# Kernel optimization log

Measured on AMD Instinct MI355X. Metric: run time of the kernel, lower is better.

The kernel has to match this reference:

```python
import jax, jax.numpy as jnp
import numpy as np

D = 1024      # model_size
H = 16        # n_heads
HD = D // H   # head_size
B = 8
S = 1024


def setup_inputs() -> dict:
    key = jax.random.key(0)
    ks = jax.random.split(key, 8)
    sq = lambda k, shp: jax.random.normal(k, shp, dtype=jnp.float32) * (1.0 / np.sqrt(shp[0]))
    return {
        "query": jax.random.normal(ks[0], (B, S, D), dtype=jnp.float32),
        "value": jax.random.normal(ks[1], (B, S, D), dtype=jnp.float32),
        "Wq": sq(ks[2], (D, D)),
        "bq": jnp.zeros((D,), dtype=jnp.float32),
        "Wkv": sq(ks[3], (D, 2 * D)),
        "bkv": jnp.zeros((2 * D,), dtype=jnp.float32),
        "Wo": sq(ks[4], (D, D)),
        "bo": jnp.zeros((D,), dtype=jnp.float32),
    }


def reference(query, value, Wq, bq, Wkv, bkv, Wo, bo):
    scale = 1.0 / jnp.sqrt(jnp.float32(HD))
    q = query @ Wq + bq                      # [B,S,D]
    kv = value @ Wkv + bkv                   # [B,S,2D]
    # tf.split(kv, 2H): chunks 0..H-1 are K heads, H..2H-1 are V heads
    k = kv[..., :D].reshape(B, S, H, HD)
    v = kv[..., D:].reshape(B, S, H, HD)
    qh = q.reshape(B, S, H, HD)
    scores = jnp.einsum("bqhd,bkhd->bhqk", qh, k) * scale   # [B,H,S,S]
    attn = jax.nn.softmax(scores, axis=-1)
    heads = jnp.einsum("bhqk,bkhd->bqhd", attn, v).reshape(B, S, D)
    return heads @ Wo + bo
```

## Files before the change

### kernel.cpp

```cpp
#include <hip/hip_runtime.h>
#include <math.h>

#define B_  8
#define S_  1024
#define D_  1024
#define H_  16
#define HD_ 64

typedef float          floatx4  __attribute__((ext_vector_type(4)));
typedef __bf16         bf16x8   __attribute__((ext_vector_type(8)));
typedef unsigned int   uintx2   __attribute__((ext_vector_type(2)));
typedef unsigned int   uintx4   __attribute__((ext_vector_type(4)));

__device__ __forceinline__ unsigned short f2bf(float f) {
    union { float f; unsigned u; } v; v.f = f;
    unsigned r = v.u + 0x7FFFu + ((v.u >> 16) & 1u);
    return (unsigned short)(r >> 16);
}
__device__ __forceinline__ unsigned pk2(float a, float b) {
    union { __bf16 h[2]; unsigned u; } r;
    r.h[0] = (__bf16)a; r.h[1] = (__bf16)b;
    return r.u;
}
__device__ __forceinline__ void async16(const void* g, void* l) {
    __builtin_amdgcn_global_load_lds(
        (__attribute__((address_space(1))) void*)g,
        (__attribute__((address_space(3))) void*)l, 16, 0, 0);
}

__global__ __launch_bounds__(256) void prep_k(const float* __restrict__ query,
                                              const float* __restrict__ value,
                                              unsigned short* __restrict__ qbf,
                                              unsigned short* __restrict__ vbf,
                                              const float* __restrict__ Wq,
                                              const float* __restrict__ Wkv,
                                              const float* __restrict__ Wo,
                                              unsigned short* __restrict__ WqT,
                                              unsigned short* __restrict__ WkvT,
                                              unsigned short* __restrict__ WoT) {
    __shared__ float T[64 * 68];
    const int t   = threadIdx.x;
    const int bid = blockIdx.x;
    if (bid < 8192) {
        int i = bid * 256 + t;
        floatx4 a = ((const floatx4*)query)[i];
        floatx4 b = ((const floatx4*)value)[i];
        uintx2 oa = { pk2(a[0], a[1]), pk2(a[2], a[3]) };
        uintx2 ob = { pk2(b[0], b[1]), pk2(b[2], b[3]) };
        ((uintx2*)qbf)[i] = oa;
        ((uintx2*)vbf)[i] = ob;
        return;
    }
    const int lin = bid - 8192;
    const int z   = lin >> 8;
    const float* W; unsigned short* WT; int Ndim, nbase;
    if (z == 0)      { W = Wq;  WT = WqT;  Ndim = 1024; nbase = 0; }
    else if (z == 3) { W = Wo;  WT = WoT;  Ndim = 1024; nbase = 0; }
    else             { W = Wkv; WT = WkvT; Ndim = 2048; nbase = (z - 1) * 1024; }
    const int n0 = (lin & 15) * 64 + nbase;
    const int k0 = ((lin >> 4) & 15) * 64;
#pragma unroll
    for (int rep = 0; rep < 4; ++rep) {
        int kl = (t >> 4) + rep * 16;
        int ns = (t & 15) * 4;
        *(floatx4*)(T + kl * 68 + ns) = *(const floatx4*)(W + (size_t)(k0 + kl) * Ndim + n0 + ns);
    }
    __syncthreads();
#pragma unroll
    for (int rep = 0; rep < 2; ++rep) {
        int nl = (t >> 3) + rep * 32;
        int ks = (t & 7) * 8;
        union { unsigned short s[8]; uintx4 u; } o;
#pragma unroll
        for (int j = 0; j < 8; ++j) o.s[j] = f2bf(T[(ks + j) * 68 + nl]);
        *(uintx4*)(WT + (size_t)(n0 + nl) * 1024 + k0 + ks) = o.u;
    }
}

template<int SWAP>
__device__ __forceinline__ void kloop(const unsigned short* __restrict__ ga0,
                                      const unsigned short* __restrict__ gb0,
                                      unsigned short* __restrict__ As,
                                      unsigned short* __restrict__ Bs,
                                      floatx4 (&acc)[4][4],
                                      int w, int lane) {
    const int quad = lane >> 4;
    const int l15  = lane & 15;
    const int e7   = l15 & 7;
    const int wr   = (w >> 1) * 64;
    const int wc   = (w & 1) * 64;
    for (int k0 = 0; k0 < 1024; k0 += 64) {
        if (k0) __syncthreads();
#pragma unroll
        for (int i = 0; i < 4; ++i) {
            int c = i * 4 + w;
            async16(ga0 + (size_t)(c * 8) * 1024 + k0, As + c * 512);
            async16(gb0 + (size_t)(c * 8) * 1024 + k0, Bs + c * 512);
        }
        __syncthreads();
#pragma unroll
        for (int ks = 0; ks < 2; ++ks) {
            bf16x8 af[4], bf[4];
#pragma unroll
            for (int mi = 0; mi < 4; ++mi)
                af[mi] = *(const bf16x8*)(As + (wr + mi * 16 + l15) * 64 + (((ks * 4 + quad) ^ e7) * 8));
#pragma unroll
            for (int ni = 0; ni < 4; ++ni)
                bf[ni] = *(const bf16x8*)(Bs + (wc + ni * 16 + l15) * 64 + (((ks * 4 + quad) ^ e7) * 8));
#pragma unroll
            for (int mi = 0; mi < 4; ++mi)
#pragma unroll
                for (int ni = 0; ni < 4; ++ni)
                    acc[mi][ni] = SWAP
                        ? __builtin_amdgcn_mfma_f32_16x16x32_bf16(bf[ni], af[mi], acc[mi][ni], 0, 0, 0)
                        : __builtin_amdgcn_mfma_f32_16x16x32_bf16(af[mi], bf[ni], acc[mi][ni], 0, 0, 0);
        }
    }
}

__global__ __launch_bounds__(256, 4) void qkv_gemm_k(const unsigned short* __restrict__ qbf,
                                                     const unsigned short* __restrict__ vbf,
                                                     const unsigned short* __restrict__ WqT,
                                                     const unsigned short* __restrict__ WkvT,
                                                     const float* __restrict__ bq,
                                                     const float* __restrict__ bkv,
                                                     unsigned short* __restrict__ Qb,
                                                     unsigned short* __restrict__ Kb,
                                                     unsigned short* __restrict__ Vtg,
                                                     float cexp) {
    __shared__ unsigned short SMEM[2 * 128 * 64];
    unsigned short* As = SMEM;
    unsigned short* Bs = SMEM + 128 * 64;
    const int t    = threadIdx.x;
    const int lane = t & 63;
    const int w    = t >> 6;
    const int quad = lane >> 4;
    const int l15  = lane & 15;
    const int wr   = (w >> 1) * 64;
    const int wc   = (w & 1) * 64;
    const int lrow = lane >> 3;
    const int lswz = ((lane & 7) ^ lrow) * 8;

    const int swz = (blockIdx.x & 7) * 192 + (blockIdx.x >> 3);
    int m0, n0;
    const unsigned short *Ap, *Wp;
    const float* bp;
    unsigned short* outp;
    float sc;
    bool vpath = false;
    if (swz < 512) {
        m0 = (swz >> 3) * 128; n0 = (swz & 7) * 128;
        Ap = qbf; Wp = WqT; bp = bq; outp = Qb; sc = cexp;
    } else {
        int b2 = swz - 512;
        m0 = (b2 >> 4) * 128; n0 = (b2 & 15) * 128;
        Ap = vbf; Wp = WkvT; bp = bkv; outp = Kb; sc = 1.0f;
        vpath = (n0 >= 1024);
    }

    floatx4 acc[4][4] = {};
    const unsigned short* ga0 = Ap + (size_t)(m0 + lrow) * 1024 + lswz;
    const unsigned short* gb0 = Wp + (size_t)(n0 + lrow) * 1024 + lswz;

    if (!vpath) {
        kloop<1>(ga0, gb0, As, Bs, acc, w, lane);
        __syncthreads();
#pragma unroll
        for (int hn = 0; hn < 2; ++hn) {
            if ((w & 1) == hn) {
#pragma unroll
                for (int ni = 0; ni < 4; ++ni) {
                    const int nb = n0 + wc + ni * 16 + quad * 4;
                    const floatx4 b4 = *(const floatx4*)(bp + nb);
#pragma unroll
                    for (int mi = 0; mi < 4; ++mi) {
                        const int ml = wr + mi * 16 + l15;
                        floatx4 v = acc[mi][ni];
                        uintx2 o = { pk2((v[0] + b4[0]) * sc, (v[1] + b4[1]) * sc),
                                     pk2((v[2] + b4[2]) * sc, (v[3] + b4[3]) * sc) };
                        *(uintx2*)(SMEM + ml * 72 + ni * 16 + quad * 4) = o;
                    }
                }
            }
            __syncthreads();
#pragma unroll
            for (int p = 0; p < 4; ++p) {
                int u   = p * 256 + t;
                int row = u >> 3, ch = u & 7;
                uintx4 x = *(const uintx4*)(SMEM + row * 72 + ch * 8);
                *(uintx4*)(outp + (size_t)(m0 + row) * 1024 + (n0 & 1023) + hn * 64 + ch * 8) = x;
            }
            __syncthreads();
        }
    } else {
        kloop<0>(ga0, gb0, As, Bs, acc, w, lane);
        const int c0 = n0 - 1024;
        const int s0 = m0 & 1023;
        const int bb = m0 >> 10;
        __syncthreads();
#pragma unroll
        for (int hc = 0; hc < 2; ++hc) {
            if ((w & 1) == hc) {
#pragma unroll
                for (int ni = 0; ni < 4; ++ni) {
                    const int rl = ni * 16 + l15;
                    const float bv = bp[n0 + wc + ni * 16 + l15];
#pragma unroll
                    for (int mi = 0; mi < 4; ++mi) {
                        const int sl = wr + mi * 16 + quad * 4;
                        floatx4 v = acc[mi][ni];
                        uintx2 o = { pk2(v[0] + bv, v[1] + bv), pk2(v[2] + bv, v[3] + bv) };
                        *(uintx2*)(SMEM + rl * 136 + sl) = o;
                    }
                }
            }
            __syncthreads();
#pragma unroll
            for (int p = 0; p < 4; ++p) {
                int u   = p * 256 + t;
                int row = u >> 4, ch = u & 15;
                uintx4 x = *(const uintx4*)(SMEM + row * 136 + ch * 8);
                *(uintx4*)(Vtg + ((size_t)(bb * 1024 + c0 + hc * 64 + row)) * 1024 + s0 + ch * 8) = x;
            }
            __syncthreads();
        }
    }
}

__global__ __launch_bounds__(256, 4) void o_gemm_k(const unsigned short* __restrict__ Hb,
                                                   const unsigned short* __restrict__ WoT,
                                                   const float* __restrict__ bo,
                                                   float* __restrict__ out) {
    __shared__ unsigned short As[128 * 64];
    __shared__ unsigned short Bs[128 * 64];
    const int t    = threadIdx.x;
    const int lane = t & 63;
    const int w    = t >> 6;
    const int quad = lane >> 4;
    const int l15  = lane & 15;
    const int wr   = (w >> 1) * 64;
    const int wc   = (w & 1) * 64;
    const int lrow = lane >> 3;
    const int lswz = ((lane & 7) ^ lrow) * 8;
    const int swz = (blockIdx.x & 7) * 64 + (blockIdx.x >> 3);
    const int m0  = (swz >> 3) * 128;
    const int n0  = (swz & 7) * 128;

    floatx4 acc[4][4] = {};
    const unsigned short* ga0 = Hb  + (size_t)(m0 + lrow) * 1024 + lswz;
    const unsigned short* gb0 = WoT + (size_t)(n0 + lrow) * 1024 + lswz;
    kloop<1>(ga0, gb0, As, Bs, acc, w, lane);

#pragma unroll
    for (int ni = 0; ni < 4; ++ni) {
        const int nb = n0 + wc + ni * 16 + quad * 4;
        const floatx4 b4 = *(const floatx4*)(bo + nb);
#pragma unroll
        for (int mi = 0; mi < 4; ++mi) {
            const int m = m0 + wr + mi * 16 + l15;
            floatx4 v = acc[mi][ni];
            floatx4 o = { v[0] + b4[0], v[1] + b4[1], v[2] + b4[2], v[3] + b4[3] };
            *(floatx4*)(out + (size_t)m * 1024 + nb) = o;
        }
    }
}

__global__ __launch_bounds__(512, 4) void attn_kernel(const unsigned short* __restrict__ Qb,
                                                      const unsigned short* __restrict__ Kb,
                                                      const unsigned short* __restrict__ Vtg,
                                                      unsigned short* __restrict__ Hb) {
    __shared__ unsigned short QPs[256 * 64];
    __shared__ unsigned short Ks[2][64 * 64];
    __shared__ unsigned short Vs[2][64 * 64];

    const int lin = blockIdx.x;
    const int xcd = lin & 7;
    const int grp = lin >> 3;
    const int bh  = xcd * 16 + (grp >> 2);
    const int qt  = grp & 3;
    const int b   = bh >> 4;
    const int h   = bh & 15;
    const int q0  = qt * 256;

    const int t    = threadIdx.x;
    const int lane = t & 63;
    const int w    = t >> 6;
    const int quad = lane >> 4;
    const int l15  = lane & 15;
    const int e7   = l15 & 7;
    const int lrow = lane >> 3;
    const int lswz = ((lane & 7) ^ lrow) * 8;

    {
        const unsigned short* gq = Qb + ((size_t)(b * S_ + q0)) * D_ + h * HD_;
#pragma unroll
        for (int i = 0; i < 4; ++i) {
            int r0 = (w * 4 + i) * 8;
            async16(gq + (size_t)(r0 + lrow) * D_ + lswz, QPs + r0 * 64);
        }
    }
    __syncthreads();

    bf16x8 bQ[2][2];
#pragma unroll
    for (int ks = 0; ks < 2; ++ks)
#pragma unroll
        for (int ni = 0; ni < 2; ++ni)
            bQ[ks][ni] = *(const bf16x8*)(QPs + (w * 32 + ni * 16 + l15) * 64 + ((ks * 4 + quad) ^ e7) * 8);

    const unsigned short* gkbase = Kb  + ((size_t)b * S_) * D_ + h * HD_;
    const unsigned short* gvbase = Vtg + ((size_t)(b * D_ + h * HD_)) * S_;

    float   lsum[2] = { 0.f, 0.f };
    floatx4 oacc[4][2] = {};
    unsigned short* Psw = QPs + w * (32 * 64);

    auto stageK = [&](int kt, int buf) {
        int r0 = w * 8;
        async16(gkbase + (size_t)(kt * 64 + r0 + lrow) * D_ + lswz, &Ks[buf][r0 * 64]);
    };
    auto stageV = [&](int kt, int buf) {
        int r0 = w * 8;
        async16(gvbase + (size_t)(r0 + lrow) * S_ + kt * 64 + lswz, &Vs[buf][r0 * 64]);
    };

    stageK(0, 0);
    stageV(0, 0);

#pragma unroll 1
    for (int kt = 0; kt < 16; ++kt) {
        const int cur = kt & 1;
        asm volatile("s_waitcnt vmcnt(0)\n\ts_barrier" ::: "memory");
        if (kt < 15) { stageK(kt + 1, cur ^ 1); stageV(kt + 1, cur ^ 1); }

        floatx4 st[4][2] = {};
#pragma unroll
        for (int ks = 0; ks < 2; ++ks) {
            bf16x8 aK[4];
#pragma unroll
            for (int mi = 0; mi < 4; ++mi)
                aK[mi] = *(const bf16x8*)(&Ks[cur][0] + (mi * 16 + l15) * 64 + ((ks * 4 + quad) ^ e7) * 8);
            __builtin_amdgcn_s_setprio(1);
#pragma unroll
            for (int mi = 0; mi < 4; ++mi)
#pragma unroll
                for (int ni = 0; ni < 2; ++ni)
                    st[mi][ni] = __builtin_amdgcn_mfma_f32_16x16x32_bf16(aK[mi], bQ[ks][ni], st[mi][ni], 0, 0, 0);
            __builtin_amdgcn_s_setprio(0);
        }

#pragma unroll
        for (int ni = 0; ni < 2; ++ni) {
            float ls = 0.f;
#pragma unroll
            for (int mi = 0; mi < 4; ++mi) {
                float p0 = __builtin_amdgcn_exp2f(st[mi][ni][0]);
                float p1 = __builtin_amdgcn_exp2f(st[mi][ni][1]);
                float p2 = __builtin_amdgcn_exp2f(st[mi][ni][2]);
                float p3 = __builtin_amdgcn_exp2f(st[mi][ni][3]);
                ls += (p0 + p1) + (p2 + p3);
                uintx2 pk = { pk2(p0, p1), pk2(p2, p3) };
                *(uintx2*)(Psw + (ni * 16 + l15) * 64 +
                           (((2 * mi + (quad >> 1)) ^ e7) * 8 + (quad & 1) * 4)) = pk;
            }
            lsum[ni] += ls;
        }

#pragma unroll
        for (int ks = 0; ks < 2; ++ks) {
            bf16x8 aV[4], bP[2];
#pragma unroll
            for (int mi = 0; mi < 4; ++mi)
                aV[mi] = *(const bf16x8*)(&Vs[cur][0] + (mi * 16 + l15) * 64 + ((ks * 4 + quad) ^ e7) * 8);
#pragma unroll
            for (int ni = 0; ni < 2; ++ni)
                bP[ni] = *(const bf16x8*)(Psw + (ni * 16 + l15) * 64 + ((ks * 4 + quad) ^ e7) * 8);
            __builtin_amdgcn_s_setprio(1);
#pragma unroll
            for (int mi = 0; mi < 4; ++mi)
#pragma unroll
                for (int ni = 0; ni < 2; ++ni)
                    oacc[mi][ni] = __builtin_amdgcn_mfma_f32_16x16x32_bf16(aV[mi], bP[ni], oacc[mi][ni], 0, 0, 0);
            __builtin_amdgcn_s_setprio(0);
        }
    }

    float rl[2];
#pragma unroll
    for (int ni = 0; ni < 2; ++ni) {
        float l = lsum[ni];
        l += __shfl_xor(l, 16);
        l += __shfl_xor(l, 32);
        rl[ni] = 1.f / l;
    }
#pragma unroll
    for (int mi = 0; mi < 4; ++mi)
#pragma unroll
        for (int ni = 0; ni < 2; ++ni) {
            uintx2 pk = { pk2(oacc[mi][ni][0] * rl[ni], oacc[mi][ni][1] * rl[ni]),
                          pk2(oacc[mi][ni][2] * rl[ni], oacc[mi][ni][3] * rl[ni]) };
            *(uintx2*)(Psw + (ni * 16 + l15) * 64 +
                       (((2 * mi + (quad >> 1)) ^ e7) * 8 + (quad & 1) * 4)) = pk;
        }
    {
        int qrow = lane >> 1;
        int kh   = lane & 1;
        size_t obase = ((size_t)(b * S_ + q0 + w * 32 + qrow)) * D_ + h * HD_ + kh * 32;
        int e = qrow & 7;
#pragma unroll
        for (int j = 0; j < 4; ++j) {
            int chunk = kh * 4 + j;
            *(uintx4*)(Hb + obase + j * 8) =
                *(const uintx4*)(Psw + qrow * 64 + ((chunk ^ e) * 8));
        }
    }
}

extern "C" void kernel_launch(void* const* d_in, const int* in_sizes, int n_in,
                              void* d_out, int out_size, void* d_ws, size_t ws_size,
                              hipStream_t stream) {
    (void)in_sizes; (void)n_in; (void)out_size; (void)ws_size;
    const float* query = (const float*)d_in[0];
    const float* value = (const float*)d_in[1];
    const float* Wq    = (const float*)d_in[2];
    const float* bq    = (const float*)d_in[3];
    const float* Wkv   = (const float*)d_in[4];
    const float* bkv   = (const float*)d_in[5];
    const float* Wo    = (const float*)d_in[6];
    const float* bo    = (const float*)d_in[7];

    const size_t MS = (size_t)B_ * S_;
    char* p = (char*)d_ws;
    unsigned short* qbf  = (unsigned short*)p; p += MS * D_ * 2;
    unsigned short* vbf  = (unsigned short*)p; p += MS * D_ * 2;
    unsigned short* WqT  = (unsigned short*)p; p += (size_t)D_ * D_ * 2;
    unsigned short* WkvT = (unsigned short*)p; p += (size_t)2 * D_ * D_ * 2;
    unsigned short* WoT  = (unsigned short*)p; p += (size_t)D_ * D_ * 2;
    unsigned short* Qb   = (unsigned short*)p; p += MS * D_ * 2;
    unsigned short* Kb   = (unsigned short*)p; p += MS * D_ * 2;
    unsigned short* Vtg  = (unsigned short*)p; p += MS * D_ * 2;
    unsigned short* Hb   = qbf;

    const float cexp = 0.125f * 1.44269504088896341f;

    prep_k<<<9216, 256, 0, stream>>>(query, value, qbf, vbf, Wq, Wkv, Wo, WqT, WkvT, WoT);
    qkv_gemm_k<<<1536, 256, 0, stream>>>(qbf, vbf, WqT, WkvT, bq, bkv, Qb, Kb, Vtg, cexp);
    attn_kernel<<<512, 512, 0, stream>>>(Qb, Kb, Vtg, Hb);
    o_gemm_k<<<512, 256, 0, stream>>>(Hb, WoT, bo, (float*)d_out);
}
```

Baseline: 262.8 us.

## Fuse fp32-to-bf16 activation cast into QKV GEMM A-tile loads

Drops the separate pass that casts query and value to bf16. The QKV GEMM now reads fp32 activations directly and converts them in registers before writing the A tile to LDS, so the bf16 copies are never written out and read back. The block-to-tile mapping also changes from a swizzled order to m-fastest ordering in both GEMMs. The trade-off is that the A-tile load becomes a synchronous register load plus conversion instead of an async global-to-LDS copy, and each A tile is fetched from global memory at twice the byte size, once per N tile.

Measured after the change: 267.6 us. No clear change (+1.8%).

```diff
diff --git a/kernel.cpp b/kernel.cpp
--- a/kernel.cpp
+++ b/kernel.cpp
@@ -28,11 +28,7 @@
         (__attribute__((address_space(3))) void*)l, 16, 0, 0);
 }
 
-__global__ __launch_bounds__(256) void prep_k(const float* __restrict__ query,
-                                              const float* __restrict__ value,
-                                              unsigned short* __restrict__ qbf,
-                                              unsigned short* __restrict__ vbf,
-                                              const float* __restrict__ Wq,
+__global__ __launch_bounds__(256) void prep_k(const float* __restrict__ Wq,
                                               const float* __restrict__ Wkv,
                                               const float* __restrict__ Wo,
                                               unsigned short* __restrict__ WqT,
@@ -40,18 +36,7 @@
                                               unsigned short* __restrict__ WoT) {
     __shared__ float T[64 * 68];
     const int t   = threadIdx.x;
-    const int bid = blockIdx.x;
-    if (bid < 8192) {
-        int i = bid * 256 + t;
-        floatx4 a = ((const floatx4*)query)[i];
-        floatx4 b = ((const floatx4*)value)[i];
-        uintx2 oa = { pk2(a[0], a[1]), pk2(a[2], a[3]) };
-        uintx2 ob = { pk2(b[0], b[1]), pk2(b[2], b[3]) };
-        ((uintx2*)qbf)[i] = oa;
-        ((uintx2*)vbf)[i] = ob;
-        return;
-    }
-    const int lin = bid - 8192;
+    const int lin = blockIdx.x;
     const int z   = lin >> 8;
     const float* W; unsigned short* WT; int Ndim, nbase;
     if (z == 0)      { W = Wq;  WT = WqT;  Ndim = 1024; nbase = 0; }
@@ -77,8 +62,9 @@
     }
 }
 
-template<int SWAP>
+template<int SWAP, int CASTA>
 __device__ __forceinline__ void kloop(const unsigned short* __restrict__ ga0,
+                                      const float* __restrict__ gaf,
                                       const unsigned short* __restrict__ gb0,
                                       unsigned short* __restrict__ As,
                                       unsigned short* __restrict__ Bs,
@@ -94,8 +80,30 @@
 #pragma unroll
         for (int i = 0; i < 4; ++i) {
             int c = i * 4 + w;
-            async16(ga0 + (size_t)(c * 8) * 1024 + k0, As + c * 512);
             async16(gb0 + (size_t)(c * 8) * 1024 + k0, Bs + c * 512);
+        }
+        if constexpr (CASTA) {
+            floatx4 x[4][2];
+#pragma unroll
+            for (int i = 0; i < 4; ++i) {
+                int c = i * 4 + w;
+                const float* src = gaf + (size_t)(c * 8) * 1024 + k0;
+                x[i][0] = *(const floatx4*)(src);
+                x[i][1] = *(const floatx4*)(src + 4);
+            }
+#pragma unroll
+            for (int i = 0; i < 4; ++i) {
+                int c = i * 4 + w;
+                uintx4 o = { pk2(x[i][0][0], x[i][0][1]), pk2(x[i][0][2], x[i][0][3]),
+                             pk2(x[i][1][0], x[i][1][1]), pk2(x[i][1][2], x[i][1][3]) };
+                *(uintx4*)(As + c * 512 + lane * 8) = o;
+            }
+        } else {
+#pragma unroll
+            for (int i = 0; i < 4; ++i) {
+                int c = i * 4 + w;
+                async16(ga0 + (size_t)(c * 8) * 1024 + k0, As + c * 512);
+            }
         }
         __syncthreads();
 #pragma unroll
@@ -118,8 +126,8 @@
     }
 }
 
-__global__ __launch_bounds__(256, 4) void qkv_gemm_k(const unsigned short* __restrict__ qbf,
-                                                     const unsigned short* __restrict__ vbf,
+__global__ __launch_bounds__(256, 4) void qkv_gemm_k(const float* __restrict__ query,
+                                                     const float* __restrict__ value,
                                                      const unsigned short* __restrict__ WqT,
                                                      const unsigned short* __restrict__ WkvT,
                                                      const float* __restrict__ bq,
@@ -141,29 +149,30 @@
     const int lrow = lane >> 3;
     const int lswz = ((lane & 7) ^ lrow) * 8;
 
-    const int swz = (blockIdx.x & 7) * 192 + (blockIdx.x >> 3);
+    const int bid = blockIdx.x;
     int m0, n0;
-    const unsigned short *Ap, *Wp;
+    const float* Af;
+    const unsigned short* Wp;
     const float* bp;
     unsigned short* outp;
     float sc;
     bool vpath = false;
-    if (swz < 512) {
-        m0 = (swz >> 3) * 128; n0 = (swz & 7) * 128;
-        Ap = qbf; Wp = WqT; bp = bq; outp = Qb; sc = cexp;
+    if (bid < 512) {
+        m0 = (bid & 63) * 128; n0 = (bid >> 6) * 128;
+        Af = query; Wp = WqT; bp = bq; outp = Qb; sc = cexp;
     } else {
-        int b2 = swz - 512;
-        m0 = (b2 >> 4) * 128; n0 = (b2 & 15) * 128;
-        Ap = vbf; Wp = WkvT; bp = bkv; outp = Kb; sc = 1.0f;
+        int b2 = bid - 512;
+        m0 = (b2 & 63) * 128; n0 = (b2 >> 6) * 128;
+        Af = value; Wp = WkvT; bp = bkv; outp = Kb; sc = 1.0f;
         vpath = (n0 >= 1024);
     }
 
     floatx4 acc[4][4] = {};
-    const unsigned short* ga0 = Ap + (size_t)(m0 + lrow) * 1024 + lswz;
+    const float* gaf          = Af + (size_t)(m0 + lrow) * 1024 + lswz;
     const unsigned short* gb0 = Wp + (size_t)(n0 + lrow) * 1024 + lswz;
 
     if (!vpath) {
-        kloop<1>(ga0, gb0, As, Bs, acc, w, lane);
+        kloop<1, 1>(nullptr, gaf, gb0, As, Bs, acc, w, lane);
         __syncthreads();
 #pragma unroll
         for (int hn = 0; hn < 2; ++hn) {
@@ -193,7 +202,7 @@
             __syncthreads();
         }
     } else {
-        kloop<0>(ga0, gb0, As, Bs, acc, w, lane);
+        kloop<0, 1>(nullptr, gaf, gb0, As, Bs, acc, w, lane);
         const int c0 = n0 - 1024;
         const int s0 = m0 & 1023;
         const int bb = m0 >> 10;
@@ -242,14 +251,13 @@
     const int wc   = (w & 1) * 64;
     const int lrow = lane >> 3;
     const int lswz = ((lane & 7) ^ lrow) * 8;
-    const int swz = (blockIdx.x & 7) * 64 + (blockIdx.x >> 3);
-    const int m0  = (swz >> 3) * 128;
-    const int n0  = (swz & 7) * 128;
+    const int m0   = (blockIdx.x & 63) * 128;
+    const int n0   = (blockIdx.x >> 6) * 128;
 
     floatx4 acc[4][4] = {};
     const unsigned short* ga0 = Hb  + (size_t)(m0 + lrow) * 1024 + lswz;
     const unsigned short* gb0 = WoT + (size_t)(n0 + lrow) * 1024 + lswz;
-    kloop<1>(ga0, gb0, As, Bs, acc, w, lane);
+    kloop<1, 0>(ga0, nullptr, gb0, As, Bs, acc, w, lane);
 
 #pragma unroll
     for (int ni = 0; ni < 4; ++ni) {
@@ -431,20 +439,18 @@
 
     const size_t MS = (size_t)B_ * S_;
     char* p = (char*)d_ws;
-    unsigned short* qbf  = (unsigned short*)p; p += MS * D_ * 2;
-    unsigned short* vbf  = (unsigned short*)p; p += MS * D_ * 2;
     unsigned short* WqT  = (unsigned short*)p; p += (size_t)D_ * D_ * 2;
     unsigned short* WkvT = (unsigned short*)p; p += (size_t)2 * D_ * D_ * 2;
     unsigned short* WoT  = (unsigned short*)p; p += (size_t)D_ * D_ * 2;
     unsigned short* Qb   = (unsigned short*)p; p += MS * D_ * 2;
     unsigned short* Kb   = (unsigned short*)p; p += MS * D_ * 2;
     unsigned short* Vtg  = (unsigned short*)p; p += MS * D_ * 2;
-    unsigned short* Hb   = qbf;
+    unsigned short* Hb   = (unsigned short*)p; p += MS * D_ * 2;
 
     const float cexp = 0.125f * 1.44269504088896341f;
 
-    prep_k<<<9216, 256, 0, stream>>>(query, value, qbf, vbf, Wq, Wkv, Wo, WqT, WkvT, WoT);
-    qkv_gemm_k<<<1536, 256, 0, stream>>>(qbf, vbf, WqT, WkvT, bq, bkv, Qb, Kb, Vtg, cexp);
+    prep_k<<<1024, 256, 0, stream>>>(Wq, Wkv, Wo, WqT, WkvT, WoT);
+    qkv_gemm_k<<<1536, 256, 0, stream>>>(query, value, WqT, WkvT, bq, bkv, Qb, Kb, Vtg, cexp);
     attn_kernel<<<512, 512, 0, stream>>>(Qb, Kb, Vtg, Hb);
     o_gemm_k<<<512, 256, 0, stream>>>(Hb, WoT, bo, (float*)d_out);
 }
```
